# Optimization experiments

Hardware: AMD Instinct MI355X
Metric: run time of the kernel (lower is better)

Reference implementation:

```python
import jax, jax.numpy as jnp
import numpy as np

N, H, E = 50000, 128, 1600000

def setup_inputs() -> dict:
    key = jax.random.key(0)
    k1, k2, k3, k4 = jax.random.split(key, 4)
    h = jax.random.normal(k1, (N, H), dtype=jnp.float32)
    edge_index = jax.random.randint(k2, (2, E), 0, N, dtype=jnp.int64)
    # edge_scorer: Linear(2H, 1); node_scorer: Linear(H, 1)
    W_edge = jax.random.normal(k3, (2 * H, 1), dtype=jnp.float32) / np.sqrt(2 * H)
    b_edge = jnp.zeros((1,), dtype=jnp.float32)
    W_node = jax.random.normal(k4, (H, 1), dtype=jnp.float32) / np.sqrt(H)
    b_node = jnp.zeros((1,), dtype=jnp.float32)
    return {"h": h, "edge_index": edge_index, "W_edge": W_edge,
            "b_edge": b_edge, "W_node": W_node, "b_node": b_node}

def reference(h, edge_index, W_edge, b_edge, W_node, b_node):
    n = h.shape[0]
    src, dst = edge_index[0], edge_index[1]
    # cat([h[src], h[dst]]) @ W_edge == (h @ W_src)[src] + (h @ W_dst)[dst]
    # (same math as the torch module, avoids materializing the (E, 2H) concat)
    W_src, W_dst = W_edge[:h.shape[1]], W_edge[h.shape[1]:]
    s_src = (h @ W_src)[:, 0]            # (N,)
    s_dst = (h @ W_dst)[:, 0]            # (N,)
    edge_scores = s_src[src] + s_dst[dst] + b_edge[0]   # (E,)
    node_edge_score = jax.ops.segment_sum(edge_scores, dst, num_segments=n)
    node_self_score = (h @ W_node)[:, 0] + b_node[0]    # (N,)
    combined = node_edge_score + node_self_score
    return jax.nn.softmax(combined, axis=0)
```

## Files before the change

### kernel.cpp

```cpp
#include <hip/hip_runtime.h>
#include <math.h>


#define RANGE_BITS 14
#define RANGE_SIZE (1 << RANGE_BITS)
#define NCHUNKS 64

__device__ __forceinline__ void atomicMaxFloat(float* addr, float val) {
    if (val >= 0.0f) atomicMax((int*)addr, __float_as_int(val));
    else             atomicMin((unsigned int*)addr, __float_as_uint(val));
}

__global__ __launch_bounds__(256) void node_scores_kernel(
    const float* __restrict__ h,
    const float* __restrict__ W_edge,
    const float* __restrict__ b_edge,
    const float* __restrict__ W_node,
    const float* __restrict__ b_node,
    float* __restrict__ s_src,
    float* __restrict__ t_dst,
    float* __restrict__ self_sc,
    float* __restrict__ acc,
    float* __restrict__ gmax,
    float* __restrict__ gsum,
    int N, int H)
{
    if (blockIdx.x == 0 && threadIdx.x == 0) { *gmax = -INFINITY; *gsum = 0.0f; }

    const int lane16 = threadIdx.x & 15;
    const int n = (blockIdx.x * blockDim.x + threadIdx.x) >> 4;
    if (n >= N) return;

    const float4* __restrict__ h4  = (const float4*)(h + (size_t)n * H);
    const float4* __restrict__ ws4 = (const float4*)(W_edge);
    const float4* __restrict__ wd4 = (const float4*)(W_edge + H);
    const float4* __restrict__ wn4 = (const float4*)(W_node);
    const int H4 = H >> 2;

    float ps = 0.0f, pd = 0.0f, pn = 0.0f;
    for (int i = lane16; i < H4; i += 16) {
        float4 hv = h4[i];
        float4 a = ws4[i], b = wd4[i], c = wn4[i];
        ps = fmaf(hv.x, a.x, fmaf(hv.y, a.y, fmaf(hv.z, a.z, fmaf(hv.w, a.w, ps))));
        pd = fmaf(hv.x, b.x, fmaf(hv.y, b.y, fmaf(hv.z, b.z, fmaf(hv.w, b.w, pd))));
        pn = fmaf(hv.x, c.x, fmaf(hv.y, c.y, fmaf(hv.z, c.z, fmaf(hv.w, c.w, pn))));
    }
    #pragma unroll
    for (int off = 8; off > 0; off >>= 1) {
        ps += __shfl_xor(ps, off, 64);
        pd += __shfl_xor(pd, off, 64);
        pn += __shfl_xor(pn, off, 64);
    }
    if (lane16 == 0) {
        float self = pn + b_node[0];
        s_src[n]   = ps;
        t_dst[n]   = pd + b_edge[0];
        self_sc[n] = self;
        acc[n]     = self;
    }
}

__global__ __launch_bounds__(1024) void edge_bin_kernel(
    const int* __restrict__ ei,
    const float* __restrict__ s_src,
    const float* __restrict__ t_dst,
    float* __restrict__ partials,
    int N, int E, int chunk, int vec_ok)
{
    __shared__ float hist[RANGE_SIZE];
    const int b  = blockIdx.x;
    const int r  = blockIdx.y;
    const int lo = r << RANGE_BITS;
    const int hi = min(lo + RANGE_SIZE, N);

    for (int i = threadIdx.x; i < RANGE_SIZE; i += blockDim.x) hist[i] = 0.0f;
    __syncthreads();

    const int e0 = b * chunk;
    const int e1 = min(e0 + chunk, E);
    if (e0 < e1) {
        if (vec_ok) {
            const int nvec = (e1 - e0) >> 2;
            const int4* __restrict__ dst4 = (const int4*)(ei + E + e0);
            for (int i = threadIdx.x; i < nvec; i += blockDim.x) {
                int4 d = dst4[i];
                const int eb = e0 + 4 * i;
                if (d.x >= lo && d.x < hi) atomicAdd(&hist[d.x - lo], s_src[ei[eb + 0]] + t_dst[d.x]);
                if (d.y >= lo && d.y < hi) atomicAdd(&hist[d.y - lo], s_src[ei[eb + 1]] + t_dst[d.y]);
                if (d.z >= lo && d.z < hi) atomicAdd(&hist[d.z - lo], s_src[ei[eb + 2]] + t_dst[d.z]);
                if (d.w >= lo && d.w < hi) atomicAdd(&hist[d.w - lo], s_src[ei[eb + 3]] + t_dst[d.w]);
            }
            for (int e = e0 + 4 * nvec + threadIdx.x; e < e1; e += blockDim.x) {
                int d = ei[E + e];
                if (d >= lo && d < hi) atomicAdd(&hist[d - lo], s_src[ei[e]] + t_dst[d]);
            }
        } else {
            for (int e = e0 + threadIdx.x; e < e1; e += blockDim.x) {
                int d = ei[E + e];
                if (d >= lo && d < hi) atomicAdd(&hist[d - lo], s_src[ei[e]] + t_dst[d]);
            }
        }
    }
    __syncthreads();

    float* __restrict__ outp = partials + (size_t)b * N + lo;
    const int len = hi - lo;
    if ((len & 3) == 0) {
        const int len4 = len >> 2;
        const float4* __restrict__ h4 = (const float4*)hist;
        float4* __restrict__ o4 = (float4*)outp;
        for (int i = threadIdx.x; i < len4; i += blockDim.x) o4[i] = h4[i];
    } else {
        for (int i = threadIdx.x; i < len; i += blockDim.x) outp[i] = hist[i];
    }
}

__global__ __launch_bounds__(256) void edge_accum_fallback_kernel(
    const int* __restrict__ ei,
    const float* __restrict__ s_src,
    const float* __restrict__ t_dst,
    float* __restrict__ acc,
    int E)
{
    int e = blockIdx.x * blockDim.x + threadIdx.x;
    if (e >= E) return;
    int s = ei[e];
    int d = ei[E + e];
    atomicAdd(&acc[d], s_src[s] + t_dst[d]);
}

__device__ __forceinline__ float blockReduceMaxB(float v) {
    __shared__ float sm[16];
    #pragma unroll
    for (int off = 32; off > 0; off >>= 1) v = fmaxf(v, __shfl_xor(v, off, 64));
    const int w = threadIdx.x >> 6, l = threadIdx.x & 63;
    const int nw = blockDim.x >> 6;
    if (l == 0) sm[w] = v;
    __syncthreads();
    float r = sm[0];
    for (int i = 1; i < nw; ++i) r = fmaxf(r, sm[i]);
    __syncthreads();
    return r;
}

__device__ __forceinline__ float blockReduceSumB(float v) {
    __shared__ float sm[16];
    #pragma unroll
    for (int off = 32; off > 0; off >>= 1) v += __shfl_xor(v, off, 64);
    const int w = threadIdx.x >> 6, l = threadIdx.x & 63;
    const int nw = blockDim.x >> 6;
    if (l == 0) sm[w] = v;
    __syncthreads();
    float r = 0.0f;
    for (int i = 0; i < nw; ++i) r += sm[i];
    __syncthreads();
    return r;
}

__global__ __launch_bounds__(256) void combine_max_kernel(
    const float* __restrict__ self_sc,
    const float* __restrict__ partials,
    float* __restrict__ acc,
    float* __restrict__ gmax,
    int N, int B, int use_partials)
{
    float m = -INFINITY;
    for (int i = blockIdx.x * blockDim.x + threadIdx.x; i < N;
         i += gridDim.x * blockDim.x) {
        float v;
        if (use_partials) {
            float v0 = self_sc[i], v1 = 0.0f, v2 = 0.0f, v3 = 0.0f;
            int b = 0;
            for (; b + 4 <= B; b += 4) {
                v0 += partials[(size_t)(b + 0) * N + i];
                v1 += partials[(size_t)(b + 1) * N + i];
                v2 += partials[(size_t)(b + 2) * N + i];
                v3 += partials[(size_t)(b + 3) * N + i];
            }
            for (; b < B; ++b) v0 += partials[(size_t)b * N + i];
            v = (v0 + v1) + (v2 + v3);
            acc[i] = v;
        } else {
            v = acc[i];
        }
        m = fmaxf(m, v);
    }
    m = blockReduceMaxB(m);
    if (threadIdx.x == 0) atomicMaxFloat(gmax, m);
}

__global__ __launch_bounds__(256) void exp_sum_kernel(
    const float* __restrict__ acc, const float* __restrict__ gmax,
    float* __restrict__ out, float* __restrict__ gsum, int N)
{
    const float mx = *gmax;
    float s = 0.0f;
    for (int i = blockIdx.x * blockDim.x + threadIdx.x; i < N;
         i += gridDim.x * blockDim.x) {
        float v = __expf(acc[i] - mx);
        out[i] = v;
        s += v;
    }
    s = blockReduceSumB(s);
    if (threadIdx.x == 0) atomicAdd(gsum, s);
}

__global__ __launch_bounds__(256) void normalize_kernel(
    float* __restrict__ out, const float* __restrict__ gsum, int N)
{
    int i = blockIdx.x * blockDim.x + threadIdx.x;
    if (i >= N) return;
    out[i] *= (1.0f / *gsum);
}

extern "C" void kernel_launch(void* const* d_in, const int* in_sizes, int n_in,
                              void* d_out, int out_size, void* d_ws, size_t ws_size,
                              hipStream_t stream) {
    const float* h      = (const float*)d_in[0];
    const int*   ei     = (const int*)  d_in[1];
    const float* W_edge = (const float*)d_in[2];
    const float* b_edge = (const float*)d_in[3];
    const float* W_node = (const float*)d_in[4];
    const float* b_node = (const float*)d_in[5];

    const int H = in_sizes[2] / 2;
    const int N = in_sizes[0] / H;
    const int E = in_sizes[1] / 2;

    float* out      = (float*)d_out;
    float* ws       = (float*)d_ws;
    float* s_src    = ws;
    float* t_dst    = ws + (size_t)N;
    float* self_s   = ws + 2 * (size_t)N;
    float* acc      = ws + 3 * (size_t)N;
    float* gmax     = ws + 4 * (size_t)N;
    float* gsum     = ws + 4 * (size_t)N + 1;
    float* partials = ws + 4 * (size_t)N + 2;

    const size_t base_floats = 4 * (size_t)N + 2;
    int B = 0;
    if (ws_size / sizeof(float) > base_floats) {
        size_t avail = ws_size / sizeof(float) - base_floats;
        B = (int)(avail / (size_t)N);
    }
    if (B > NCHUNKS) B = NCHUNKS;
    const int R = (N + RANGE_SIZE - 1) >> RANGE_BITS;
    const int use_partials = (B >= 16) ? 1 : 0;

    {
        int threads = N * 16;
        int grid = (threads + 255) / 256;
        node_scores_kernel<<<grid, 256, 0, stream>>>(
            h, W_edge, b_edge, W_node, b_node,
            s_src, t_dst, self_s, acc, gmax, gsum, N, H);
    }
    if (use_partials) {
        int chunk = (((E + B - 1) / B) + 3) & ~3;
        int vec_ok = ((E & 3) == 0) ? 1 : 0;
        dim3 grid(B, R);
        edge_bin_kernel<<<grid, 1024, 0, stream>>>(
            ei, s_src, t_dst, partials, N, E, chunk, vec_ok);
    } else {
        int grid = (E + 255) / 256;
        edge_accum_fallback_kernel<<<grid, 256, 0, stream>>>(ei, s_src, t_dst, acc, E);
    }
    combine_max_kernel<<<256, 256, 0, stream>>>(
        self_s, partials, acc, gmax, N, B, use_partials);
    {
        int grid = (N + 255) / 256;
        exp_sum_kernel<<<grid, 256, 0, stream>>>(acc, gmax, out, gsum, N);
        normalize_kernel<<<grid, 256, 0, stream>>>(out, gsum, N);
    }
}
```

Baseline: 120.9 us.

## Fuse softmax stages with online max/sum and per-block partial stats

```diff
diff --git a/kernel.cpp b/kernel.cpp
--- a/kernel.cpp
+++ b/kernel.cpp
@@ -5,11 +5,7 @@
 #define RANGE_BITS 14
 #define RANGE_SIZE (1 << RANGE_BITS)
 #define NCHUNKS 64
-
-__device__ __forceinline__ void atomicMaxFloat(float* addr, float val) {
-    if (val >= 0.0f) atomicMax((int*)addr, __float_as_int(val));
-    else             atomicMin((unsigned int*)addr, __float_as_uint(val));
-}
+#define STAT_BLOCKS 256
 
 __global__ __launch_bounds__(256) void node_scores_kernel(
     const float* __restrict__ h,
@@ -21,12 +17,8 @@
     float* __restrict__ t_dst,
     float* __restrict__ self_sc,
     float* __restrict__ acc,
-    float* __restrict__ gmax,
-    float* __restrict__ gsum,
     int N, int H)
 {
-    if (blockIdx.x == 0 && threadIdx.x == 0) { *gmax = -INFINITY; *gsum = 0.0f; }
-
     const int lane16 = threadIdx.x & 15;
     const int n = (blockIdx.x * blockDim.x + threadIdx.x) >> 4;
     if (n >= N) return;
@@ -72,6 +64,7 @@
     const int r  = blockIdx.y;
     const int lo = r << RANGE_BITS;
     const int hi = min(lo + RANGE_SIZE, N);
+    const unsigned span = (unsigned)(hi - lo);
 
     for (int i = threadIdx.x; i < RANGE_SIZE; i += blockDim.x) hist[i] = 0.0f;
     __syncthreads();
@@ -85,19 +78,23 @@
             for (int i = threadIdx.x; i < nvec; i += blockDim.x) {
                 int4 d = dst4[i];
                 const int eb = e0 + 4 * i;
-                if (d.x >= lo && d.x < hi) atomicAdd(&hist[d.x - lo], s_src[ei[eb + 0]] + t_dst[d.x]);
-                if (d.y >= lo && d.y < hi) atomicAdd(&hist[d.y - lo], s_src[ei[eb + 1]] + t_dst[d.y]);
-                if (d.z >= lo && d.z < hi) atomicAdd(&hist[d.z - lo], s_src[ei[eb + 2]] + t_dst[d.z]);
-                if (d.w >= lo && d.w < hi) atomicAdd(&hist[d.w - lo], s_src[ei[eb + 3]] + t_dst[d.w]);
+                unsigned ux = (unsigned)(d.x - lo), uy = (unsigned)(d.y - lo);
+                unsigned uz = (unsigned)(d.z - lo), uw = (unsigned)(d.w - lo);
+                if (ux < span) atomicAdd(&hist[ux], s_src[ei[eb + 0]] + t_dst[d.x]);
+                if (uy < span) atomicAdd(&hist[uy], s_src[ei[eb + 1]] + t_dst[d.y]);
+                if (uz < span) atomicAdd(&hist[uz], s_src[ei[eb + 2]] + t_dst[d.z]);
+                if (uw < span) atomicAdd(&hist[uw], s_src[ei[eb + 3]] + t_dst[d.w]);
             }
             for (int e = e0 + 4 * nvec + threadIdx.x; e < e1; e += blockDim.x) {
                 int d = ei[E + e];
-                if (d >= lo && d < hi) atomicAdd(&hist[d - lo], s_src[ei[e]] + t_dst[d]);
+                unsigned u = (unsigned)(d - lo);
+                if (u < span) atomicAdd(&hist[u], s_src[ei[e]] + t_dst[d]);
             }
         } else {
             for (int e = e0 + threadIdx.x; e < e1; e += blockDim.x) {
                 int d = ei[E + e];
-                if (d >= lo && d < hi) atomicAdd(&hist[d - lo], s_src[ei[e]] + t_dst[d]);
+                unsigned u = (unsigned)(d - lo);
+                if (u < span) atomicAdd(&hist[u], s_src[ei[e]] + t_dst[d]);
             }
         }
     }
@@ -157,14 +154,14 @@
     return r;
 }
 
-__global__ __launch_bounds__(256) void combine_max_kernel(
+__global__ __launch_bounds__(256) void combine_stats_kernel(
     const float* __restrict__ self_sc,
     const float* __restrict__ partials,
     float* __restrict__ acc,
-    float* __restrict__ gmax,
+    float* __restrict__ red,
     int N, int B, int use_partials)
 {
-    float m = -INFINITY;
+    float m = -INFINITY, l = 0.0f;
     for (int i = blockIdx.x * blockDim.x + threadIdx.x; i < N;
          i += gridDim.x * blockDim.x) {
         float v;
@@ -183,34 +180,33 @@
         } else {
             v = acc[i];
         }
-        m = fmaxf(m, v);
-    }
-    m = blockReduceMaxB(m);
-    if (threadIdx.x == 0) atomicMaxFloat(gmax, m);
-}
-
-__global__ __launch_bounds__(256) void exp_sum_kernel(
-    const float* __restrict__ acc, const float* __restrict__ gmax,
-    float* __restrict__ out, float* __restrict__ gsum, int N)
-{
-    const float mx = *gmax;
-    float s = 0.0f;
-    for (int i = blockIdx.x * blockDim.x + threadIdx.x; i < N;
-         i += gridDim.x * blockDim.x) {
-        float v = __expf(acc[i] - mx);
-        out[i] = v;
-        s += v;
-    }
-    s = blockReduceSumB(s);
-    if (threadIdx.x == 0) atomicAdd(gsum, s);
-}
-
-__global__ __launch_bounds__(256) void normalize_kernel(
-    float* __restrict__ out, const float* __restrict__ gsum, int N)
-{
+        float nm = fmaxf(m, v);
+        l = l * __expf(m - nm) + __expf(v - nm);
+        m = nm;
+    }
+    float mb = blockReduceMaxB(m);
+    float ladj = (m == -INFINITY) ? 0.0f : l * __expf(m - mb);
+    float lb = blockReduceSumB(ladj);
+    if (threadIdx.x == 0) {
+        red[blockIdx.x] = mb;
+        red[STAT_BLOCKS + blockIdx.x] = lb;
+    }
+}
+
+__global__ __launch_bounds__(256) void finalize_kernel(
+    const float* __restrict__ acc,
+    const float* __restrict__ red,
+    float* __restrict__ out,
+    int N)
+{
+    float m = red[threadIdx.x];
+    float l = red[STAT_BLOCKS + threadIdx.x];
+    float M = blockReduceMaxB(m);
+    float L = blockReduceSumB(l * __expf(m - M));
+    const float inv = 1.0f / L;
+
     int i = blockIdx.x * blockDim.x + threadIdx.x;
-    if (i >= N) return;
-    out[i] *= (1.0f / *gsum);
+    if (i < N) out[i] = __expf(acc[i] - M) * inv;
 }
 
 extern "C" void kernel_launch(void* const* d_in, const int* in_sizes, int n_in,
@@ -233,11 +229,10 @@
     float* t_dst    = ws + (size_t)N;
     float* self_s   = ws + 2 * (size_t)N;
     float* acc      = ws + 3 * (size_t)N;
-    float* gmax     = ws + 4 * (size_t)N;
-    float* gsum     = ws + 4 * (size_t)N + 1;
-    float* partials = ws + 4 * (size_t)N + 2;
-
-    const size_t base_floats = 4 * (size_t)N + 2;
+    float* red      = ws + 4 * (size_t)N;
+    float* partials = red + 2 * STAT_BLOCKS;
+
+    const size_t base_floats = 4 * (size_t)N + 2 * STAT_BLOCKS;
     int B = 0;
     if (ws_size / sizeof(float) > base_floats) {
         size_t avail = ws_size / sizeof(float) - base_floats;
@@ -252,7 +247,7 @@
         int grid = (threads + 255) / 256;
         node_scores_kernel<<<grid, 256, 0, stream>>>(
             h, W_edge, b_edge, W_node, b_node,
-            s_src, t_dst, self_s, acc, gmax, gsum, N, H);
+            s_src, t_dst, self_s, acc, N, H);
     }
     if (use_partials) {
         int chunk = (((E + B - 1) / B) + 3) & ~3;
@@ -264,11 +259,10 @@
         int grid = (E + 255) / 256;
         edge_accum_fallback_kernel<<<grid, 256, 0, stream>>>(ei, s_src, t_dst, acc, E);
     }
-    combine_max_kernel<<<256, 256, 0, stream>>>(
-        self_s, partials, acc, gmax, N, B, use_partials);
+    combine_stats_kernel<<<STAT_BLOCKS, 256, 0, stream>>>(
+        self_s, partials, acc, red, N, B, use_partials);
     {
         int grid = (N + 255) / 256;
-        exp_sum_kernel<<<grid, 256, 0, stream>>>(acc, gmax, out, gsum, N);
-        normalize_kernel<<<grid, 256, 0, stream>>>(out, gsum, N);
-    }
-}
+        finalize_kernel<<<grid, 256, 0, stream>>>(acc, red, out, N);
+    }
+}
```

Result: faster. 115.5 us (-4.4%).
